# Optimization experiments

Hardware: AMD Instinct MI355X
Metric: run time of the kernel (lower is better)

## Reference

```python
import jax, jax.numpy as jnp
import numpy as np

BN_EPS = 1e-5
THRESH = 0.81


def _prelu(x, w):
    return jnp.where(x >= 0, x, w * x)


def setup_inputs() -> dict:
    key = jax.random.key(0)
    k1, = jax.random.split(key, 1)
    B, F, L = 8, 2048, 1024
    x = jax.random.normal(k1, (B, F, L), dtype=jnp.float32)
    # PReLU weights (default num_parameters=1, init=0.25)
    prelu1_w = jnp.full((1,), 0.25, dtype=jnp.float32)
    prelu2_w = jnp.full((1,), 0.25, dtype=jnp.float32)
    # BatchNorm1d(nfeat) affine params (default init weight=1, bias=0)
    bn_weight = jnp.ones((F,), dtype=jnp.float32)
    bn_bias = jnp.zeros((F,), dtype=jnp.float32)
    return {"x": x, "prelu1_w": prelu1_w, "prelu2_w": prelu2_w,
            "bn_weight": bn_weight, "bn_bias": bn_bias}


def reference(x, prelu1_w, prelu2_w, bn_weight, bn_bias):
    # x: [B, F, L]
    B, F, L = x.shape
    # --- Adj_Dynamic: PReLU -> AdaptiveAvgPool1d(1) -> BatchNorm1d (training-mode batch stats)
    h = _prelu(x, prelu1_w)                       # [B, F, L]
    h = jnp.mean(h, axis=-1, keepdims=True)       # [B, F, 1]
    mu = jnp.mean(h, axis=(0, 2), keepdims=True)  # per-channel mean over (B, L=1)
    var = jnp.mean((h - mu) ** 2, axis=(0, 2), keepdims=True)  # biased variance
    h = (h - mu) * jax.lax.rsqrt(var + BN_EPS)
    h = h * bn_weight[None, :, None] + bn_bias[None, :, None]  # [B, F, 1]
    # --- dynamic adjacency
    sim = jnp.einsum('bni,bmi->bnm', h, h)        # [B, F, F]
    I = jnp.eye(F, dtype=x.dtype)
    A = jnp.where(sim > THRESH, 1.0, 0.0) + I     # [B, F, F]
    # --- symmetric degree normalization D^-1/2 A D^-1/2 (diag matmuls as row/col scaling)
    d_inv_sqrt = jnp.sum(A, axis=-1) ** -0.5      # [B, F]
    A_hat = d_inv_sqrt[:, :, None] * A * d_inv_sqrt[:, None, :]
    # --- output PReLU
    return _prelu(A_hat, prelu2_w)
```

## Files before the change

### kernel.cpp

```cpp
#include <hip/hip_runtime.h>

#define B 8
#define F 2048
#define L 1024
#define BN_EPS 1e-5f
#define THRESH 0.81f

__global__ __launch_bounds__(256) void pool_kernel(const float* __restrict__ x,
                                                   const float* __restrict__ p1,
                                                   float* __restrict__ h) {
    const int wave = threadIdx.x >> 6;
    const int lane = threadIdx.x & 63;
    const int row  = blockIdx.x * 4 + wave;
    const float w = p1[0];
    const float4* xr = (const float4*)(x + (size_t)row * L);
    float sum = 0.f;
#pragma unroll
    for (int k = 0; k < 4; ++k) {
        float4 v = xr[lane + 64 * k];
        sum += (v.x >= 0.f) ? v.x : w * v.x;
        sum += (v.y >= 0.f) ? v.y : w * v.y;
        sum += (v.z >= 0.f) ? v.z : w * v.z;
        sum += (v.w >= 0.f) ? v.w : w * v.w;
    }
#pragma unroll
    for (int off = 32; off > 0; off >>= 1)
        sum += __shfl_down(sum, off, 64);
    if (lane == 0) h[row] = sum * (1.0f / L);
}

__global__ __launch_bounds__(256) void bn_kernel(float* __restrict__ h,
                                                 const float* __restrict__ bnw,
                                                 const float* __restrict__ bnb) {
    const int f = blockIdx.x * 256 + threadIdx.x;
    float v[B];
    float mu = 0.f;
#pragma unroll
    for (int b = 0; b < B; ++b) { v[b] = h[b * F + f]; mu += v[b]; }
    mu *= (1.0f / B);
    float var = 0.f;
#pragma unroll
    for (int b = 0; b < B; ++b) { float d = v[b] - mu; var += d * d; }
    var *= (1.0f / B);
    const float scale = (1.0f / sqrtf(var + BN_EPS)) * bnw[f];
    const float bias  = bnb[f];
#pragma unroll
    for (int b = 0; b < B; ++b) h[b * F + f] = (v[b] - mu) * scale + bias;
}

__global__ __launch_bounds__(256) void deg_kernel(const float* __restrict__ hn,
                                                  float* __restrict__ dinv) {
    __shared__ float sh[F];
    __shared__ int partial[4][64];
    const int b    = blockIdx.x / (F / 64);
    const int nblk = blockIdx.x % (F / 64);
    for (int i = threadIdx.x; i < F; i += 256) sh[i] = hn[b * F + i];
    __syncthreads();
    const int nl = threadIdx.x & 63;
    const int q  = threadIdx.x >> 6;
    const int n  = nblk * 64 + nl;
    const float hv = sh[n];
    int cnt = 0;
    const int m0 = q * (F / 4);
    for (int m = 0; m < F / 4; m += 4) {
        float4 hm = *(const float4*)&sh[m0 + m];
        cnt += (hv * hm.x > THRESH);
        cnt += (hv * hm.y > THRESH);
        cnt += (hv * hm.z > THRESH);
        cnt += (hv * hm.w > THRESH);
    }
    partial[q][nl] = cnt;
    __syncthreads();
    if (q == 0) {
        int deg = 1 + partial[0][nl] + partial[1][nl] + partial[2][nl] + partial[3][nl];
        dinv[b * F + n] = 1.0f / sqrtf((float)deg);
    }
}

__global__ __launch_bounds__(256) void out_kernel(const float* __restrict__ hn,
                                                  const float* __restrict__ dinv,
                                                  const float* __restrict__ p2,
                                                  float* __restrict__ out) {
    const int row = blockIdx.x;
    const int n   = row & (F - 1);
    const int bF  = row & ~(F - 1);
    const float hv = hn[row];
    const float dn = dinv[row];
    const float w2 = p2[0];
    const float4* hm4 = (const float4*)(hn + bF);
    const float4* dm4 = (const float4*)(dinv + bF);
    float4* o4 = (float4*)(out + (size_t)row * F);
    for (int t = threadIdx.x; t < F / 4; t += 256) {
        float4 hm = hm4[t];
        float4 dm = dm4[t];
        const int m = t * 4;
        float4 r;
        {
            float a = (hv * hm.x > THRESH) ? 1.f : 0.f; if (n == m + 0) a += 1.f;
            float v = (dn * a) * dm.x; r.x = (v >= 0.f) ? v : w2 * v;
        }
        {
            float a = (hv * hm.y > THRESH) ? 1.f : 0.f; if (n == m + 1) a += 1.f;
            float v = (dn * a) * dm.y; r.y = (v >= 0.f) ? v : w2 * v;
        }
        {
            float a = (hv * hm.z > THRESH) ? 1.f : 0.f; if (n == m + 2) a += 1.f;
            float v = (dn * a) * dm.z; r.z = (v >= 0.f) ? v : w2 * v;
        }
        {
            float a = (hv * hm.w > THRESH) ? 1.f : 0.f; if (n == m + 3) a += 1.f;
            float v = (dn * a) * dm.w; r.w = (v >= 0.f) ? v : w2 * v;
        }
        o4[t] = r;
    }
}

extern "C" void kernel_launch(void* const* d_in, const int* in_sizes, int n_in,
                              void* d_out, int out_size, void* d_ws, size_t ws_size,
                              hipStream_t stream) {
    const float* x   = (const float*)d_in[0];
    const float* p1  = (const float*)d_in[1];
    const float* p2  = (const float*)d_in[2];
    const float* bnw = (const float*)d_in[3];
    const float* bnb = (const float*)d_in[4];
    float* out = (float*)d_out;

    float* h    = (float*)d_ws;
    float* dinv = h + B * F;

    pool_kernel<<<(B * F) / 4, 256, 0, stream>>>(x, p1, h);
    bn_kernel<<<F / 256, 256, 0, stream>>>(h, bnw, bnb);
    deg_kernel<<<B * (F / 64), 256, 0, stream>>>(h, dinv);
    out_kernel<<<B * F, 256, 0, stream>>>(h, dinv, p2, out);
}
```

Before: 194.3 us.

## Fuse pooling with batchnorm, process multiple output rows per block, use nontemporal memory ops

Pooling and BatchNorm are merged into one kernel in which each block owns one feature channel across all batches, which removes a launch and the round trip of h through global memory. The output kernel now computes 8 rows per block, so each hn/dinv load is reused across rows, and it writes with nontemporal stores. The x reads also become nontemporal loads. The cost is that the fused kernel reads x with strided rows, and the BN step runs serially on a single thread.

```diff
diff --git a/kernel.cpp b/kernel.cpp
--- a/kernel.cpp
+++ b/kernel.cpp
@@ -6,46 +6,50 @@
 #define BN_EPS 1e-5f
 #define THRESH 0.81f
 
-__global__ __launch_bounds__(256) void pool_kernel(const float* __restrict__ x,
-                                                   const float* __restrict__ p1,
-                                                   float* __restrict__ h) {
+typedef float nt4 __attribute__((ext_vector_type(4)));
+
+__global__ __launch_bounds__(256) void poolbn_kernel(const float* __restrict__ x,
+                                                     const float* __restrict__ p1,
+                                                     const float* __restrict__ bnw,
+                                                     const float* __restrict__ bnb,
+                                                     float* __restrict__ h) {
+    __shared__ float hh[B];
+    const int f    = blockIdx.x;
     const int wave = threadIdx.x >> 6;
     const int lane = threadIdx.x & 63;
-    const int row  = blockIdx.x * 4 + wave;
-    const float w = p1[0];
-    const float4* xr = (const float4*)(x + (size_t)row * L);
-    float sum = 0.f;
+    const float w  = p1[0];
 #pragma unroll
-    for (int k = 0; k < 4; ++k) {
-        float4 v = xr[lane + 64 * k];
-        sum += (v.x >= 0.f) ? v.x : w * v.x;
-        sum += (v.y >= 0.f) ? v.y : w * v.y;
-        sum += (v.z >= 0.f) ? v.z : w * v.z;
-        sum += (v.w >= 0.f) ? v.w : w * v.w;
+    for (int b = wave; b < B; b += 4) {
+        const nt4* xr = (const nt4*)(x + ((size_t)b * F + f) * L);
+        float sum = 0.f;
+#pragma unroll
+        for (int k = 0; k < 4; ++k) {
+            nt4 v = __builtin_nontemporal_load(&xr[lane + 64 * k]);
+            sum += (v.x >= 0.f) ? v.x : w * v.x;
+            sum += (v.y >= 0.f) ? v.y : w * v.y;
+            sum += (v.z >= 0.f) ? v.z : w * v.z;
+            sum += (v.w >= 0.f) ? v.w : w * v.w;
+        }
+#pragma unroll
+        for (int off = 32; off > 0; off >>= 1)
+            sum += __shfl_down(sum, off, 64);
+        if (lane == 0) hh[b] = sum * (1.0f / L);
     }
+    __syncthreads();
+    if (threadIdx.x == 0) {
+        float mu = 0.f;
 #pragma unroll
-    for (int off = 32; off > 0; off >>= 1)
-        sum += __shfl_down(sum, off, 64);
-    if (lane == 0) h[row] = sum * (1.0f / L);
-}
-
-__global__ __launch_bounds__(256) void bn_kernel(float* __restrict__ h,
-                                                 const float* __restrict__ bnw,
-                                                 const float* __restrict__ bnb) {
-    const int f = blockIdx.x * 256 + threadIdx.x;
-    float v[B];
-    float mu = 0.f;
+        for (int b = 0; b < B; ++b) mu += hh[b];
+        mu *= (1.0f / B);
+        float var = 0.f;
 #pragma unroll
-    for (int b = 0; b < B; ++b) { v[b] = h[b * F + f]; mu += v[b]; }
-    mu *= (1.0f / B);
-    float var = 0.f;
+        for (int b = 0; b < B; ++b) { float d = hh[b] - mu; var += d * d; }
+        var *= (1.0f / B);
+        const float scale = (1.0f / sqrtf(var + BN_EPS)) * bnw[f];
+        const float bias  = bnb[f];
 #pragma unroll
-    for (int b = 0; b < B; ++b) { float d = v[b] - mu; var += d * d; }
-    var *= (1.0f / B);
-    const float scale = (1.0f / sqrtf(var + BN_EPS)) * bnw[f];
-    const float bias  = bnb[f];
-#pragma unroll
-    for (int b = 0; b < B; ++b) h[b * F + f] = (v[b] - mu) * scale + bias;
+        for (int b = 0; b < B; ++b) h[b * F + f] = (hh[b] - mu) * scale + bias;
+    }
 }
 
 __global__ __launch_bounds__(256) void deg_kernel(const float* __restrict__ hn,
@@ -77,41 +81,49 @@
     }
 }
 
+#define ROWS 8
 __global__ __launch_bounds__(256) void out_kernel(const float* __restrict__ hn,
                                                   const float* __restrict__ dinv,
                                                   const float* __restrict__ p2,
                                                   float* __restrict__ out) {
-    const int row = blockIdx.x;
-    const int n   = row & (F - 1);
-    const int bF  = row & ~(F - 1);
-    const float hv = hn[row];
-    const float dn = dinv[row];
+    const int g  = blockIdx.x;
+    const int b  = g / (F / ROWS);
+    const int n0 = (g % (F / ROWS)) * ROWS;
     const float w2 = p2[0];
-    const float4* hm4 = (const float4*)(hn + bF);
-    const float4* dm4 = (const float4*)(dinv + bF);
-    float4* o4 = (float4*)(out + (size_t)row * F);
+    const float* hrow = hn + b * F;
+    const float* drow = dinv + b * F;
+    float hv[ROWS], dn[ROWS];
+#pragma unroll
+    for (int r = 0; r < ROWS; ++r) { hv[r] = hrow[n0 + r]; dn[r] = drow[n0 + r]; }
+    const float4* hm4 = (const float4*)hrow;
+    const float4* dm4 = (const float4*)drow;
+#pragma unroll
     for (int t = threadIdx.x; t < F / 4; t += 256) {
         float4 hm = hm4[t];
         float4 dm = dm4[t];
         const int m = t * 4;
-        float4 r;
-        {
-            float a = (hv * hm.x > THRESH) ? 1.f : 0.f; if (n == m + 0) a += 1.f;
-            float v = (dn * a) * dm.x; r.x = (v >= 0.f) ? v : w2 * v;
+#pragma unroll
+        for (int r = 0; r < ROWS; ++r) {
+            const int n = n0 + r;
+            nt4 rr;
+            {
+                float a = (hv[r] * hm.x > THRESH) ? 1.f : 0.f; if (n == m + 0) a += 1.f;
+                float v = (dn[r] * a) * dm.x; rr.x = (v >= 0.f) ? v : w2 * v;
+            }
+            {
+                float a = (hv[r] * hm.y > THRESH) ? 1.f : 0.f; if (n == m + 1) a += 1.f;
+                float v = (dn[r] * a) * dm.y; rr.y = (v >= 0.f) ? v : w2 * v;
+            }
+            {
+                float a = (hv[r] * hm.z > THRESH) ? 1.f : 0.f; if (n == m + 2) a += 1.f;
+                float v = (dn[r] * a) * dm.z; rr.z = (v >= 0.f) ? v : w2 * v;
+            }
+            {
+                float a = (hv[r] * hm.w > THRESH) ? 1.f : 0.f; if (n == m + 3) a += 1.f;
+                float v = (dn[r] * a) * dm.w; rr.w = (v >= 0.f) ? v : w2 * v;
+            }
+            __builtin_nontemporal_store(rr, (nt4*)(out + (size_t)(b * F + n) * F) + t);
         }
-        {
-            float a = (hv * hm.y > THRESH) ? 1.f : 0.f; if (n == m + 1) a += 1.f;
-            float v = (dn * a) * dm.y; r.y = (v >= 0.f) ? v : w2 * v;
-        }
-        {
-            float a = (hv * hm.z > THRESH) ? 1.f : 0.f; if (n == m + 2) a += 1.f;
-            float v = (dn * a) * dm.z; r.z = (v >= 0.f) ? v : w2 * v;
-        }
-        {
-            float a = (hv * hm.w > THRESH) ? 1.f : 0.f; if (n == m + 3) a += 1.f;
-            float v = (dn * a) * dm.w; r.w = (v >= 0.f) ? v : w2 * v;
-        }
-        o4[t] = r;
     }
 }
 
@@ -128,8 +140,7 @@
     float* h    = (float*)d_ws;
     float* dinv = h + B * F;
 
-    pool_kernel<<<(B * F) / 4, 256, 0, stream>>>(x, p1, h);
-    bn_kernel<<<F / 256, 256, 0, stream>>>(h, bnw, bnb);
+    poolbn_kernel<<<F, 256, 0, stream>>>(x, p1, bnw, bnb, h);
     deg_kernel<<<B * (F / 64), 256, 0, stream>>>(h, dinv);
-    out_kernel<<<B * F, 256, 0, stream>>>(h, dinv, p2, out);
+    out_kernel<<<(B * F) / ROWS, 256, 0, stream>>>(h, dinv, p2, out);
 }
```

Result: no change. 195.1 us (+0.4%).
